# Kernel optimization log

Hardware: AMD Instinct MI355X
Metric: run time of the kernel (lower is better)

Reference implementation:

```python
import jax, jax.numpy as jnp
import numpy as np

B, S, HID = 2, 2048, 1024
H, D = 16, 64
KD = H * D
RMS_EPS = 1e-5
L2_EPS = 1e-12


def setup_inputs() -> dict:
    key = jax.random.key(0)
    ks = jax.random.split(key, 9)
    w = lambda k, shape: jax.random.normal(k, shape, jnp.float32) * 0.02
    return {
        "x": jax.random.normal(ks[0], (B, S, HID), jnp.float32),
        "Wq": w(ks[1], (HID, KD)),
        "Wk": w(ks[2], (HID, KD)),
        "Wv": w(ks[3], (HID, KD)),
        "Wf": w(ks[4], (HID, KD)),
        "Wb": w(ks[5], (HID, H)),
        "A_log": jnp.log(jnp.full((H,), 8.0, jnp.float32)),
        "dt_bias": jnp.zeros((KD,), jnp.float32),
        "Wg": w(ks[6], (HID, KD)),
        "bg": jnp.zeros((KD,), jnp.float32),
        "Wo": w(ks[7], (KD, HID)),
        "norm_w": jnp.ones((D,), jnp.float32),
    }


def _l2norm(t):
    n = jnp.sqrt(jnp.sum(t * t, axis=-1, keepdims=True))
    return t / jnp.clip(n, L2_EPS)


def reference(x, Wq, Wk, Wv, Wf, Wb, A_log, dt_bias, Wg, bg, Wo, norm_w):
    b, s, _ = x.shape
    h = A_log.shape[0]
    d = norm_w.shape[0]

    q = jax.nn.silu(x @ Wq).reshape(b, s, h, d)
    k = jax.nn.silu(x @ Wk).reshape(b, s, h, d)
    v = jax.nn.silu(x @ Wv).reshape(b, s, h, d)
    g = (x @ Wf).reshape(b, s, h, d)
    beta = jax.nn.sigmoid(x @ Wb)  # [b,s,h]

    q = _l2norm(q)
    k = _l2norm(k)
    g = jax.nn.sigmoid(g - dt_bias.reshape(h, d))
    A = jnp.exp(-jnp.exp(A_log))  # [h]

    # seq-major for scan: [s, b, h, d]
    qs = jnp.moveaxis(q, 1, 0)
    kss = jnp.moveaxis(k, 1, 0)
    vs = jnp.moveaxis(v, 1, 0)
    gs = jnp.moveaxis(g, 1, 0)
    bs = jnp.moveaxis(beta, 1, 0)  # [s,b,h]

    state0 = jnp.zeros((b, h, d, d), x.dtype)

    def step(state, inp):
        q_t, k_t, v_t, g_t, b_t = inp
        o_t = jnp.einsum('bhd,bhde->bhe', q_t, state) * g_t
        state = A[None, :, None, None] * state \
            + b_t[..., None, None] * (k_t[..., :, None] * v_t[..., None, :])
        return state, o_t

    _, o = jax.lax.scan(step, state0, (qs, kss, vs, gs, bs))
    o = jnp.moveaxis(o, 0, 1)  # [b,s,h,d]

    # RMSNorm over head_dim, then gate
    o = o * jax.lax.rsqrt(jnp.mean(o * o, axis=-1, keepdims=True) + RMS_EPS) * norm_w
    gate = jax.nn.sigmoid(x @ Wg + bg).reshape(b, s, h, d)
    o = (o * gate).reshape(b, s, h * d)
    return o @ Wo
```

## Files before the change

kernel.cpp:

```cpp
#include <hip/hip_runtime.h>
#include <hip/hip_bf16.h>

typedef __hip_bfloat16 bf16;
typedef __attribute__((ext_vector_type(8))) short v8s;
typedef __attribute__((ext_vector_type(4))) short v4s;
typedef __attribute__((ext_vector_type(4))) float v4f;

#define MFMA16(a,b,c) __builtin_amdgcn_mfma_f32_16x16x32_bf16((a),(b),(c),0,0,0)
#define SCHED0() __builtin_amdgcn_sched_barrier(0)


static const size_t OFF_XBF    = 0;
static const size_t OFF_WCATT  = 8388608;
static const size_t OFF_WOT    = OFF_WCATT + 11010048;
static const size_t OFF_Y      = OFF_WOT + 2097152;
static const size_t OFF_BETA   = OFF_Y + 41943040;
static const size_t OFF_OINTRA = OFF_BETA + 262144;
static const size_t OFF_T      = OFF_OINTRA + 16777216;
static const size_t OFF_S      = OFF_T + 16777216;
static const size_t OFF_OPRE   = OFF_XBF;

__device__ __forceinline__ void gl2lds16(const bf16* g, bf16* l) {
  __builtin_amdgcn_global_load_lds(
      (const __attribute__((address_space(1))) void*)g,
      (__attribute__((address_space(3))) void*)l, 16, 0, 0);
}

__global__ __launch_bounds__(256) void cvt_x(const float* __restrict__ x, bf16* __restrict__ xb) {
  int t = blockIdx.x * 256 + threadIdx.x;
  int row = t >> 7, ch = t & 127;
  const float* src = x + (size_t)row * 1024 + ch * 8;
  v4f v0 = *(const v4f*)src;
  v4f v1 = *(const v4f*)(src + 4);
  union { bf16 h[8]; v8s s; } u;
  for (int i = 0; i < 4; ++i) { u.h[i] = __float2bfloat16(v0[i]); u.h[4+i] = __float2bfloat16(v1[i]); }
  int ch2 = (ch & ~7) | ((ch ^ row) & 7);
  *(v8s*)(xb + (size_t)row * 1024 + ch2 * 8) = u.s;
}

__global__ __launch_bounds__(256) void transpose_pack(
    const float* __restrict__ W0, const float* __restrict__ W1, const float* __restrict__ W2,
    const float* __restrict__ W3, const float* __restrict__ W4, const float* __restrict__ W5,
    bf16* __restrict__ WcatT, bf16* __restrict__ WoT)
{
  int mi = blockIdx.z;
  const float* W = (mi==0)?W0:(mi==1)?W1:(mi==2)?W2:(mi==3)?W3:(mi==4)?W4:W5;
  bf16* out = (mi < 5) ? (WcatT + (size_t)mi * 1048576) : WoT;
  __shared__ float tile[64][65];
  int c0 = blockIdx.x * 64;
  int r0 = blockIdx.y * 64;
  int l = threadIdx.x & 63, w = threadIdx.x >> 6;
  for (int i = 0; i < 16; ++i)
    tile[w + 4*i][l] = W[(size_t)(r0 + w + 4*i) * 1024 + c0 + l];
  __syncthreads();
  for (int i = 0; i < 16; ++i) {
    int orow = c0 + w + 4*i;
    int col = r0 + (((l >> 3) ^ (orow & 7)) << 3) + (l & 7);
    out[(size_t)orow * 1024 + col] = __float2bfloat16(tile[l][w + 4*i]);
  }
}

__global__ __launch_bounds__(128) void pack_wb(const float* __restrict__ Wb, bf16* __restrict__ out) {
  int j = blockIdx.x;
  int ch = threadIdx.x;
  union { bf16 h[8]; v8s s; } u;
  for (int i = 0; i < 8; ++i)
    u.h[i] = __float2bfloat16(j < 16 ? Wb[(size_t)(ch*8 + i) * 16 + j] : 0.f);
  int row = 5120 + j;
  int ch2 = (ch & ~7) | ((ch ^ row) & 7);
  *(v8s*)(out + (size_t)j * 1024 + ch2 * 8) = u.s;
}

__global__ __launch_bounds__(512, 2) void gemm_main(
    const bf16* __restrict__ A, const bf16* __restrict__ BT,
    bf16* __restrict__ Yb, const float* __restrict__ dtb,
    const float* __restrict__ bgp, float* __restrict__ betaOut)
{
  __shared__ bf16 As[2][16384];
  __shared__ bf16 Bs[2][16384];
  const int tid = threadIdx.x;
  int swz = ((int)blockIdx.x & 7) * 42 + ((int)blockIdx.x >> 3);
  const int by = swz / 21, bx = swz % 21;
  const int m0 = by * 256, n0 = bx * 256;
  const int w = tid >> 6, l = tid & 63;
  const int wr = w >> 2, wc = w & 3;
  const int lr = l & 15, lkq = l >> 4;
  const int xorv = lr & 7;
  const int c0 = ((lkq ^ xorv) << 3);
  const int c1 = (((4 + lkq) ^ xorv) << 3);
  const int arow = (wr * 128 + lr) * 64;
  const int brow = (wc * 64 + lr) * 64;

  v4f acc[8][4];
  #pragma unroll
  for (int i = 0; i < 8; ++i)
    #pragma unroll
    for (int j = 0; j < 4; ++j) acc[i][j] = (v4f){0.f,0.f,0.f,0.f};

#define STG_A(t_, half_) do { \
  gl2lds16(&A[(size_t)(m0 + (half_)*128 + (tid >> 3)) * 1024 + (t_)*64 + (tid & 7)*8], \
           &As[(t_) & 1][(half_)*8192 + tid*8]); \
  gl2lds16(&A[(size_t)(m0 + (half_)*128 + 64 + (tid >> 3)) * 1024 + (t_)*64 + (tid & 7)*8], \
           &As[(t_) & 1][(half_)*8192 + 4096 + tid*8]); \
} while(0)
#define STG_B(t_, half_) do { \
  gl2lds16(&BT[(size_t)(n0 + (half_)*128 + (tid >> 3)) * 1024 + (t_)*64 + (tid & 7)*8], \
           &Bs[(t_) & 1][(half_)*8192 + tid*8]); \
  gl2lds16(&BT[(size_t)(n0 + (half_)*128 + 64 + (tid >> 3)) * 1024 + (t_)*64 + (tid & 7)*8], \
           &Bs[(t_) & 1][(half_)*8192 + 4096 + tid*8]); \
} while(0)

  STG_B(0, 0); STG_B(0, 1); SCHED0();
  STG_A(0, 0); STG_A(0, 1); SCHED0();
  STG_B(1, 0); STG_B(1, 1); SCHED0();

  for (int t = 0; t < 16; ++t) {
    const int cur = t & 1;
    if (t == 15) { asm volatile("s_waitcnt vmcnt(0)" ::: "memory"); }
    else         { asm volatile("s_waitcnt vmcnt(4)" ::: "memory"); }
    SCHED0();
    __builtin_amdgcn_s_barrier();
    SCHED0();
    const bf16* Ab = &As[cur][0];
    const bf16* Bb = &Bs[cur][0];
    v8s bfr[4][2];
    #pragma unroll
    for (int nt = 0; nt < 4; ++nt) {
      bfr[nt][0] = *(const v8s*)(Bb + brow + nt*1024 + c0);
      bfr[nt][1] = *(const v8s*)(Bb + brow + nt*1024 + c1);
    }
#define PHASE(MT0, STAGE_STMT) do { \
    v8s a00 = *(const v8s*)(Ab + arow + (MT0)*1024 + c0); \
    v8s a01 = *(const v8s*)(Ab + arow + (MT0)*1024 + c1); \
    v8s a10 = *(const v8s*)(Ab + arow + ((MT0)+1)*1024 + c0); \
    v8s a11 = *(const v8s*)(Ab + arow + ((MT0)+1)*1024 + c1); \
    STAGE_STMT; \
    __builtin_amdgcn_s_setprio(1); \
    _Pragma("unroll") \
    for (int nt = 0; nt < 4; ++nt) { \
      acc[(MT0)][nt]   = MFMA16(a00, bfr[nt][0], acc[(MT0)][nt]); \
      acc[(MT0)][nt]   = MFMA16(a01, bfr[nt][1], acc[(MT0)][nt]); \
      acc[(MT0)+1][nt] = MFMA16(a10, bfr[nt][0], acc[(MT0)+1][nt]); \
      acc[(MT0)+1][nt] = MFMA16(a11, bfr[nt][1], acc[(MT0)+1][nt]); \
    } \
    __builtin_amdgcn_s_setprio(0); \
} while(0)
    PHASE(0, if (t + 1 < 16) STG_A(t + 1, 0));
    PHASE(2, if (t + 1 < 16) STG_A(t + 1, 1));
    SCHED0();
    __builtin_amdgcn_s_barrier();
    SCHED0();
    PHASE(4, if (t + 2 < 16) STG_B(t + 2, 0));
    PHASE(6, if (t + 2 < 16) STG_B(t + 2, 1));
#undef PHASE
  }
#undef STG_A
#undef STG_B

  const int region = (n0 + wc * 64) >> 10;
  #pragma unroll
  for (int mt = 0; mt < 8; ++mt)
    #pragma unroll
    for (int r = 0; r < 4; ++r) {
      int gm = m0 + wr * 128 + mt * 16 + lkq * 4 + r;
      float v[4];
      if (region < 2) {
        float ss = 0.f;
        #pragma unroll
        for (int nt = 0; nt < 4; ++nt) {
          float y = acc[mt][nt][r];
          float s = y / (1.f + __expf(-y));
          v[nt] = s; ss += s * s;
        }
        ss += __shfl_xor(ss, 1, 64); ss += __shfl_xor(ss, 2, 64);
        ss += __shfl_xor(ss, 4, 64); ss += __shfl_xor(ss, 8, 64);
        float inv = 1.f / fmaxf(sqrtf(ss), 1e-12f);
        #pragma unroll
        for (int nt = 0; nt < 4; ++nt) v[nt] *= inv;
      } else if (region == 2) {
        #pragma unroll
        for (int nt = 0; nt < 4; ++nt) {
          float y = acc[mt][nt][r];
          v[nt] = y / (1.f + __expf(-y));
        }
      } else if (region == 3) {
        #pragma unroll
        for (int nt = 0; nt < 4; ++nt) {
          int gn = n0 + wc * 64 + nt * 16 + lr;
          float z = acc[mt][nt][r] - dtb[gn & 1023];
          v[nt] = 1.f / (1.f + __expf(-z));
        }
      } else if (region == 4) {
        #pragma unroll
        for (int nt = 0; nt < 4; ++nt) {
          int gn = n0 + wc * 64 + nt * 16 + lr;
          float z = acc[mt][nt][r] + bgp[gn & 1023];
          v[nt] = 1.f / (1.f + __expf(-z));
        }
      } else {
        #pragma unroll
        for (int nt = 0; nt < 4; ++nt) {
          int gn = n0 + wc * 64 + nt * 16 + lr;
          if (gn < 5136)
            betaOut[(size_t)gm * 16 + (gn - 5120)] =
                1.f / (1.f + __expf(-acc[mt][nt][r]));
        }
        continue;
      }
      #pragma unroll
      for (int nt = 0; nt < 4; ++nt) {
        int gn = n0 + wc * 64 + nt * 16 + lr;
        Yb[(size_t)gm * 5120 + gn] = __float2bfloat16(v[nt]);
      }
    }
}

__global__ __launch_bounds__(256) void gemm_out(
    const bf16* __restrict__ A, const bf16* __restrict__ BT,
    float* __restrict__ Co)
{
  __shared__ bf16 As[2][8192];
  __shared__ bf16 Bs[2][8192];
  const int tid = threadIdx.x;
  int swzb = ((int)blockIdx.x & 7) * 32 + ((int)blockIdx.x >> 3);
  const int by = swzb >> 3, bx = swzb & 7;
  const int m0 = by * 128, n0 = bx * 128;
  const int w = tid >> 6, l = tid & 63;
  const int wm = (w >> 1) * 64, wn = (w & 1) * 64;
  const int lr = l & 15, lkq = l >> 4;
  const int xorv = lr & 7;
  const int c0 = ((lkq ^ xorv) << 3), c1 = (((4 + lkq) ^ xorv) << 3);
  v4f acc[4][4];
  for (int i = 0; i < 4; ++i) for (int j = 0; j < 4; ++j) acc[i][j] = (v4f){0.f,0.f,0.f,0.f};

#define STAGE(kk, buf) \
  for (int i_ = 0; i_ < 4; ++i_) { \
    int eo_ = (i_ * 256 + tid) * 8; \
    int r_ = eo_ >> 6, cc_ = eo_ & 63; \
    gl2lds16(&A[(size_t)(m0 + r_) * 1024 + (kk) + cc_], &As[buf][eo_]); \
    gl2lds16(&BT[(size_t)(n0 + r_) * 1024 + (kk) + cc_], &Bs[buf][eo_]); \
  }

  STAGE(0, 0);
  __syncthreads();
  int cur = 0;
  for (int kk = 0; kk < 1024; kk += 64) {
    if (kk + 64 < 1024) { STAGE(kk + 64, cur ^ 1); }
    v8s af[2][4], bfr[2][4];
    #pragma unroll
    for (int mt = 0; mt < 4; ++mt) {
      af[0][mt] = *(const v8s*)(&As[cur][(wm + mt*16 + lr) * 64 + c0]);
      af[1][mt] = *(const v8s*)(&As[cur][(wm + mt*16 + lr) * 64 + c1]);
      bfr[0][mt] = *(const v8s*)(&Bs[cur][(wn + mt*16 + lr) * 64 + c0]);
      bfr[1][mt] = *(const v8s*)(&Bs[cur][(wn + mt*16 + lr) * 64 + c1]);
    }
    #pragma unroll
    for (int kc = 0; kc < 2; ++kc)
      #pragma unroll
      for (int mt = 0; mt < 4; ++mt)
        #pragma unroll
        for (int nt = 0; nt < 4; ++nt)
          acc[mt][nt] = MFMA16(af[kc][mt], bfr[kc][nt], acc[mt][nt]);
    __syncthreads();
    cur ^= 1;
  }
#undef STAGE
  #pragma unroll
  for (int mt = 0; mt < 4; ++mt)
    #pragma unroll
    for (int nt = 0; nt < 4; ++nt)
      #pragma unroll
      for (int r = 0; r < 4; ++r) {
        int gm = m0 + wm + mt*16 + lkq*4 + r;
        int gn = n0 + wn + nt*16 + lr;
        Co[(size_t)gm * 1024 + gn] = acc[mt][nt][r];
      }
}

__global__ __launch_bounds__(256) void passA(
    const bf16* __restrict__ Y, const float* __restrict__ beta,
    const float* __restrict__ A_log, float* __restrict__ Ointra, float* __restrict__ T)
{
  int c = blockIdx.x, bh = blockIdx.y;
  int b = bh >> 4, h = bh & 15;
  int row0 = b * 2048 + c * 64;
  __shared__ bf16 Qs[64][72], Ks[64][72], Kt[64][72], Vt[64][72], Ps[64][72];
  __shared__ float betas[64], pw[64];
  int tid = threadIdx.x, w = tid >> 6, l = tid & 63;
  float aexp = __expf(A_log[h]);
  if (tid < 64) {
    pw[tid] = __expf(-aexp * (float)tid);
    betas[tid] = beta[(size_t)(row0 + tid) * 16 + h];
  }
  __syncthreads();
  for (int i = 0; i < 2; ++i) {
    int cid = i * 256 + tid;
    int r = cid >> 3, c8 = (cid & 7) * 8;
    size_t ybase = (size_t)(row0 + r) * 5120 + h * 64 + c8;
    v8s q8 = *(const v8s*)(&Y[ybase]);
    v8s k8 = *(const v8s*)(&Y[ybase + 1024]);
    v8s v8 = *(const v8s*)(&Y[ybase + 2048]);
    *(v8s*)(&Qs[r][c8]) = q8;
    *(v8s*)(&Ks[r][c8]) = k8;
    float coefT = pw[63 - r] * betas[r];
    const bf16* kp = (const bf16*)&k8;
    const bf16* vp = (const bf16*)&v8;
    for (int jj = 0; jj < 8; ++jj) {
      Vt[c8 + jj][r] = vp[jj];
      Kt[c8 + jj][r] = __float2bfloat16(coefT * __bfloat162float(kp[jj]));
    }
  }
  __syncthreads();
  const int lr = l & 15, lk = (l >> 4) * 8;
  v4f accP[4];
  for (int nt = 0; nt < 4; ++nt) accP[nt] = (v4f){0.f,0.f,0.f,0.f};
  for (int kc = 0; kc < 2; ++kc) {
    v8s a8 = *(const v8s*)(&Qs[w*16 + lr][kc*32 + lk]);
    for (int nt = 0; nt < 4; ++nt) {
      v8s b8 = *(const v8s*)(&Ks[nt*16 + lr][kc*32 + lk]);
      accP[nt] = MFMA16(a8, b8, accP[nt]);
    }
  }
  for (int nt = 0; nt < 4; ++nt)
    for (int r = 0; r < 4; ++r) {
      int tq = w*16 + (l>>4)*4 + r;
      int j  = nt*16 + lr;
      float v = accP[nt][r];
      float pm = (j < tq) ? v * betas[j] * pw[tq - 1 - j] : 0.f;
      Ps[tq][j] = __float2bfloat16(pm);
    }
  __syncthreads();
  v4f accO[4], accT[4];
  for (int nt = 0; nt < 4; ++nt) { accO[nt] = (v4f){0.f,0.f,0.f,0.f}; accT[nt] = (v4f){0.f,0.f,0.f,0.f}; }
  for (int kc = 0; kc < 2; ++kc) {
    v8s ap = *(const v8s*)(&Ps[w*16 + lr][kc*32 + lk]);
    v8s av = *(const v8s*)(&Vt[w*16 + lr][kc*32 + lk]);
    for (int nt = 0; nt < 4; ++nt) {
      v8s bv = *(const v8s*)(&Vt[nt*16 + lr][kc*32 + lk]);
      v8s bk = *(const v8s*)(&Kt[nt*16 + lr][kc*32 + lk]);
      accO[nt] = MFMA16(ap, bv, accO[nt]);
      accT[nt] = MFMA16(av, bk, accT[nt]);
    }
  }
  for (int nt = 0; nt < 4; ++nt)
    for (int r = 0; r < 4; ++r) {
      int row = w*16 + (l>>4)*4 + r;
      int col = nt*16 + lr;
      Ointra[(size_t)(row0 + row) * 1024 + h*64 + col] = accO[nt][r];
      T[((size_t)(bh*32 + c)) * 4096 + row*64 + col]   = accT[nt][r];
    }
}

__global__ __launch_bounds__(256) void passB(const float* __restrict__ T,
                                             bf16* __restrict__ S,
                                             const float* __restrict__ A_log)
{
  int e = blockIdx.x * 256 + threadIdx.x;
  int bh = e >> 12, i = e & 4095;
  float A64 = __expf(-__expf(A_log[bh & 15]) * 64.f);
  float s = 0.f;
  for (int c = 0; c < 32; ++c) {
    size_t base = ((size_t)(bh * 32 + c)) * 4096 + i;
    S[base] = __float2bfloat16(s);
    s = A64 * s + T[base];
  }
}

__global__ __launch_bounds__(256) void passC(
    const bf16* __restrict__ Y, const float* __restrict__ Ointra,
    const bf16* __restrict__ S, const float* __restrict__ A_log,
    const float* __restrict__ norm_w, bf16* __restrict__ opre)
{
  int c = blockIdx.x, bh = blockIdx.y;
  int b = bh >> 4, h = bh & 15;
  int row0 = b * 2048 + c * 64;
  __shared__ bf16 Qs[64][72], St[64][72];
  int tid = threadIdx.x, w = tid >> 6, l = tid & 63;
  float aexp = __expf(A_log[h]);
  for (int i = 0; i < 2; ++i) {
    int cid = i * 256 + tid;
    int r = cid >> 3, c8 = (cid & 7) * 8;
    *(v8s*)(&Qs[r][c8]) = *(const v8s*)(&Y[(size_t)(row0 + r) * 5120 + h*64 + c8]);
    *(v8s*)(&St[r][c8]) = *(const v8s*)(&S[((size_t)(bh*32 + c)) * 4096 + cid * 8]);
  }
  __syncthreads();
  const int lr = l & 15, lk = (l >> 4) * 8;
  v4f acc[4];
  for (int nt = 0; nt < 4; ++nt) acc[nt] = (v4f){0.f,0.f,0.f,0.f};
  for (int kc = 0; kc < 2; ++kc) {
    v8s a8 = *(const v8s*)(&Qs[w*16 + lr][kc*32 + lk]);
    for (int nt = 0; nt < 4; ++nt) {
      v8s b8 = *(const v8s*)(&St[nt*16 + lr][kc*32 + lk]);
      acc[nt] = MFMA16(a8, b8, acc[nt]);
    }
  }
  for (int r = 0; r < 4; ++r) {
    int tq = w*16 + (l>>4)*4 + r;
    float sc = __expf(-aexp * (float)tq);
    size_t orow = (size_t)(row0 + tq);
    float o[4];
    float ss = 0.f;
    for (int nt = 0; nt < 4; ++nt) {
      int e = nt*16 + lr;
      float v = Ointra[orow * 1024 + h*64 + e] + sc * acc[nt][r];
      float g = __bfloat162float(Y[orow * 5120 + 3072 + h*64 + e]);
      v *= g;
      o[nt] = v;
      ss += v * v;
    }
    ss += __shfl_xor(ss, 1, 64);
    ss += __shfl_xor(ss, 2, 64);
    ss += __shfl_xor(ss, 4, 64);
    ss += __shfl_xor(ss, 8, 64);
    float rms = rsqrtf(ss * (1.f/64.f) + 1e-5f);
    for (int nt = 0; nt < 4; ++nt) {
      int e = nt*16 + lr;
      float gate = __bfloat162float(Y[orow * 5120 + 4096 + h*64 + e]);
      float outv = o[nt] * rms * norm_w[e] * gate;
      int col = h*64 + ((((e >> 3)) ^ ((int)orow & 7)) << 3) + (e & 7);
      opre[orow * 1024 + col] = __float2bfloat16(outv);
    }
  }
}

extern "C" void kernel_launch(void* const* d_in, const int* in_sizes, int n_in,
                              void* d_out, int out_size, void* d_ws, size_t ws_size,
                              hipStream_t stream) {
  const float* x       = (const float*)d_in[0];
  const float* Wq      = (const float*)d_in[1];
  const float* Wk      = (const float*)d_in[2];
  const float* Wv      = (const float*)d_in[3];
  const float* Wf      = (const float*)d_in[4];
  const float* Wb      = (const float*)d_in[5];
  const float* A_log   = (const float*)d_in[6];
  const float* dt_bias = (const float*)d_in[7];
  const float* Wg      = (const float*)d_in[8];
  const float* bg      = (const float*)d_in[9];
  const float* Wo      = (const float*)d_in[10];
  const float* norm_w  = (const float*)d_in[11];

  char* ws = (char*)d_ws;
  bf16*  xb     = (bf16*)(ws + OFF_XBF);
  bf16*  wcatT  = (bf16*)(ws + OFF_WCATT);
  bf16*  woT    = (bf16*)(ws + OFF_WOT);
  bf16*  Y      = (bf16*)(ws + OFF_Y);
  float* beta   = (float*)(ws + OFF_BETA);
  float* Ointra = (float*)(ws + OFF_OINTRA);
  float* Tbuf   = (float*)(ws + OFF_T);
  bf16*  Sbuf   = (bf16*)(ws + OFF_S);
  bf16*  opre   = (bf16*)(ws + OFF_OPRE);

  cvt_x<<<2048, 256, 0, stream>>>(x, xb);
  transpose_pack<<<dim3(16, 16, 6), 256, 0, stream>>>(Wq, Wk, Wv, Wf, Wg, Wo, wcatT, woT);
  pack_wb<<<256, 128, 0, stream>>>(Wb, wcatT + (size_t)5120 * 1024);
  gemm_main<<<336, 512, 0, stream>>>(xb, wcatT, Y, dt_bias, bg, beta);
  passA<<<dim3(32, 32), 256, 0, stream>>>(Y, beta, A_log, Ointra, Tbuf);
  passB<<<512, 256, 0, stream>>>(Tbuf, Sbuf, A_log);
  passC<<<dim3(32, 32), 256, 0, stream>>>(Y, Ointra, Sbuf, A_log, norm_w, opre);
  gemm_out<<<256, 256, 0, stream>>>(opre, woT, (float*)d_out);
}
```

Baseline: 158.7 us.

## Halve GEMM K-tile to 32 and raise occupancy to four blocks per CU

The main projection GEMM now stages K-tiles of 32 instead of 64, halving LDS buffers and doubling loop iterations. The swizzle in the packed bf16 inputs changes from an 8-way to a 4-way XOR to match the narrower rows. Launch bounds request 4 blocks per CU instead of 2, aiming to hide latency through occupancy. In exchange there are more barriers per unit of work, and register pressure may spill under the tighter bound, since each thread holds a 128-float accumulator.

Measured after the change: 588.7 us. +270.9%, slower.

```diff
diff --git a/kernel.cpp b/kernel.cpp
--- a/kernel.cpp
+++ b/kernel.cpp
@@ -34,7 +34,7 @@
   v4f v1 = *(const v4f*)(src + 4);
   union { bf16 h[8]; v8s s; } u;
   for (int i = 0; i < 4; ++i) { u.h[i] = __float2bfloat16(v0[i]); u.h[4+i] = __float2bfloat16(v1[i]); }
-  int ch2 = (ch & ~7) | ((ch ^ row) & 7);
+  int ch2 = (ch & ~3) | ((ch ^ (row >> 1)) & 3);
   *(v8s*)(xb + (size_t)row * 1024 + ch2 * 8) = u.s;
 }
 
@@ -55,7 +55,10 @@
   __syncthreads();
   for (int i = 0; i < 16; ++i) {
     int orow = c0 + w + 4*i;
-    int col = r0 + (((l >> 3) ^ (orow & 7)) << 3) + (l & 7);
+    int q = l >> 3;
+    int q2 = (mi < 5) ? ((q & ~3) | ((q ^ (orow >> 1)) & 3))
+                      : ((q ^ orow) & 7);
+    int col = r0 + (q2 << 3) + (l & 7);
     out[(size_t)orow * 1024 + col] = __float2bfloat16(tile[l][w + 4*i]);
   }
 }
@@ -67,17 +70,17 @@
   for (int i = 0; i < 8; ++i)
     u.h[i] = __float2bfloat16(j < 16 ? Wb[(size_t)(ch*8 + i) * 16 + j] : 0.f);
   int row = 5120 + j;
-  int ch2 = (ch & ~7) | ((ch ^ row) & 7);
+  int ch2 = (ch & ~3) | ((ch ^ (row >> 1)) & 3);
   *(v8s*)(out + (size_t)j * 1024 + ch2 * 8) = u.s;
 }
 
-__global__ __launch_bounds__(512, 2) void gemm_main(
+__global__ __launch_bounds__(512, 4) void gemm_main(
     const bf16* __restrict__ A, const bf16* __restrict__ BT,
     bf16* __restrict__ Yb, const float* __restrict__ dtb,
     const float* __restrict__ bgp, float* __restrict__ betaOut)
 {
-  __shared__ bf16 As[2][16384];
-  __shared__ bf16 Bs[2][16384];
+  __shared__ bf16 As[2][8192];
+  __shared__ bf16 Bs[2][8192];
   const int tid = threadIdx.x;
   int swz = ((int)blockIdx.x & 7) * 42 + ((int)blockIdx.x >> 3);
   const int by = swz / 21, bx = swz % 21;
@@ -85,11 +88,9 @@
   const int w = tid >> 6, l = tid & 63;
   const int wr = w >> 2, wc = w & 3;
   const int lr = l & 15, lkq = l >> 4;
-  const int xorv = lr & 7;
-  const int c0 = ((lkq ^ xorv) << 3);
-  const int c1 = (((4 + lkq) ^ xorv) << 3);
-  const int arow = (wr * 128 + lr) * 64;
-  const int brow = (wc * 64 + lr) * 64;
+  const int cq = ((lkq ^ ((lr >> 1) & 3)) << 3);
+  const int arow0 = (wr * 128 + lr) * 32;
+  const int brow0 = (wc * 64 + lr) * 32;
 
   v4f acc[8][4];
   #pragma unroll
@@ -97,65 +98,50 @@
     #pragma unroll
     for (int j = 0; j < 4; ++j) acc[i][j] = (v4f){0.f,0.f,0.f,0.f};
 
-#define STG_A(t_, half_) do { \
-  gl2lds16(&A[(size_t)(m0 + (half_)*128 + (tid >> 3)) * 1024 + (t_)*64 + (tid & 7)*8], \
-           &As[(t_) & 1][(half_)*8192 + tid*8]); \
-  gl2lds16(&A[(size_t)(m0 + (half_)*128 + 64 + (tid >> 3)) * 1024 + (t_)*64 + (tid & 7)*8], \
-           &As[(t_) & 1][(half_)*8192 + 4096 + tid*8]); \
+#define STG(t_, buf_) do { \
+  gl2lds16(&A[(size_t)(m0 + (tid >> 2)) * 1024 + (t_)*32 + (tid & 3)*8], \
+           &As[buf_][tid*8]); \
+  gl2lds16(&A[(size_t)(m0 + 128 + (tid >> 2)) * 1024 + (t_)*32 + (tid & 3)*8], \
+           &As[buf_][4096 + tid*8]); \
+  gl2lds16(&BT[(size_t)(n0 + (tid >> 2)) * 1024 + (t_)*32 + (tid & 3)*8], \
+           &Bs[buf_][tid*8]); \
+  gl2lds16(&BT[(size_t)(n0 + 128 + (tid >> 2)) * 1024 + (t_)*32 + (tid & 3)*8], \
+           &Bs[buf_][4096 + tid*8]); \
 } while(0)
-#define STG_B(t_, half_) do { \
-  gl2lds16(&BT[(size_t)(n0 + (half_)*128 + (tid >> 3)) * 1024 + (t_)*64 + (tid & 7)*8], \
-           &Bs[(t_) & 1][(half_)*8192 + tid*8]); \
-  gl2lds16(&BT[(size_t)(n0 + (half_)*128 + 64 + (tid >> 3)) * 1024 + (t_)*64 + (tid & 7)*8], \
-           &Bs[(t_) & 1][(half_)*8192 + 4096 + tid*8]); \
-} while(0)
-
-  STG_B(0, 0); STG_B(0, 1); SCHED0();
-  STG_A(0, 0); STG_A(0, 1); SCHED0();
-  STG_B(1, 0); STG_B(1, 1); SCHED0();
-
-  for (int t = 0; t < 16; ++t) {
+
+  STG(0, 0); SCHED0();
+  STG(1, 1); SCHED0();
+
+  for (int t = 0; t < 32; ++t) {
     const int cur = t & 1;
-    if (t == 15) { asm volatile("s_waitcnt vmcnt(0)" ::: "memory"); }
+    if (t == 31) { asm volatile("s_waitcnt vmcnt(0)" ::: "memory"); }
     else         { asm volatile("s_waitcnt vmcnt(4)" ::: "memory"); }
     SCHED0();
     __builtin_amdgcn_s_barrier();
     SCHED0();
     const bf16* Ab = &As[cur][0];
     const bf16* Bb = &Bs[cur][0];
-    v8s bfr[4][2];
-    #pragma unroll
-    for (int nt = 0; nt < 4; ++nt) {
-      bfr[nt][0] = *(const v8s*)(Bb + brow + nt*1024 + c0);
-      bfr[nt][1] = *(const v8s*)(Bb + brow + nt*1024 + c1);
-    }
-#define PHASE(MT0, STAGE_STMT) do { \
-    v8s a00 = *(const v8s*)(Ab + arow + (MT0)*1024 + c0); \
-    v8s a01 = *(const v8s*)(Ab + arow + (MT0)*1024 + c1); \
-    v8s a10 = *(const v8s*)(Ab + arow + ((MT0)+1)*1024 + c0); \
-    v8s a11 = *(const v8s*)(Ab + arow + ((MT0)+1)*1024 + c1); \
-    STAGE_STMT; \
-    __builtin_amdgcn_s_setprio(1); \
-    _Pragma("unroll") \
-    for (int nt = 0; nt < 4; ++nt) { \
-      acc[(MT0)][nt]   = MFMA16(a00, bfr[nt][0], acc[(MT0)][nt]); \
-      acc[(MT0)][nt]   = MFMA16(a01, bfr[nt][1], acc[(MT0)][nt]); \
-      acc[(MT0)+1][nt] = MFMA16(a10, bfr[nt][0], acc[(MT0)+1][nt]); \
-      acc[(MT0)+1][nt] = MFMA16(a11, bfr[nt][1], acc[(MT0)+1][nt]); \
-    } \
-    __builtin_amdgcn_s_setprio(0); \
-} while(0)
-    PHASE(0, if (t + 1 < 16) STG_A(t + 1, 0));
-    PHASE(2, if (t + 1 < 16) STG_A(t + 1, 1));
+    v8s bfr[4], afr[8];
+    #pragma unroll
+    for (int nt = 0; nt < 4; ++nt)
+      bfr[nt] = *(const v8s*)(Bb + brow0 + nt*512 + cq);
+    #pragma unroll
+    for (int mt = 0; mt < 8; ++mt)
+      afr[mt] = *(const v8s*)(Ab + arow0 + mt*512 + cq);
+    asm volatile("s_waitcnt lgkmcnt(0)" ::: "memory");
     SCHED0();
     __builtin_amdgcn_s_barrier();
     SCHED0();
-    PHASE(4, if (t + 2 < 16) STG_B(t + 2, 0));
-    PHASE(6, if (t + 2 < 16) STG_B(t + 2, 1));
-#undef PHASE
-  }
-#undef STG_A
-#undef STG_B
+    if (t + 2 < 32) { STG(t + 2, cur); }
+    __builtin_amdgcn_s_setprio(1);
+    #pragma unroll
+    for (int mt = 0; mt < 8; ++mt)
+      #pragma unroll
+      for (int nt = 0; nt < 4; ++nt)
+        acc[mt][nt] = MFMA16(afr[mt], bfr[nt], acc[mt][nt]);
+    __builtin_amdgcn_s_setprio(0);
+  }
+#undef STG
 
   const int region = (n0 + wc * 64) >> 10;
   #pragma unroll
```
